# Optimization experiments

Hardware: AMD Instinct MI355X
Metric: run time of the kernel (lower is better)

The kernel has to match this reference:

```python
import jax, jax.numpy as jnp
import numpy as np

TOP_K = 2


def setup_inputs() -> dict:
    key = jax.random.key(0)
    k0, k1, k2, k3 = jax.random.split(key, 4)
    B, T, C, E, D = 4, 2048, 1024, 8, 1024  # D = 4*C*top_k//E
    x = jax.random.normal(k0, (B, T, C), dtype=jnp.float32)
    s = 1.0 / np.sqrt(C)
    w_router = jax.random.normal(k1, (C, E), dtype=jnp.float32) * s
    w1 = jax.random.normal(k2, (E, C, D), dtype=jnp.float32) * s  # c_fc.weight.T per expert
    w2 = jax.random.normal(k3, (E, D, C), dtype=jnp.float32) * (1.0 / np.sqrt(D))  # c_proj.weight.T
    return {"x": x, "w_router": w_router, "w1": w1, "w2": w2}


def reference(x, w_router, w1, w2):
    B, T, C = x.shape
    xf = x.reshape(-1, C)  # [N, C]
    logits = xf @ w_router  # [N, E]
    top_vals, top_idx = jax.lax.top_k(logits, TOP_K)  # [N, k]
    probs = jax.nn.softmax(top_vals, axis=-1)  # softmax over selected experts only
    # Dense per-expert MLP (relu^2), identical math to per-token weight gather:
    h = jnp.square(jax.nn.relu(jnp.einsum('nc,ecd->ned', xf, w1)))  # [N, E, D]
    y_all = jnp.einsum('ned,edc->nec', h, w2)  # [N, E, C]
    y_sel = jnp.take_along_axis(y_all, top_idx[:, :, None], axis=1)  # [N, k, C]
    out = jnp.sum(y_sel * probs[:, :, None], axis=1)  # [N, C]
    return out.reshape(B, T, C)
```

## Files before the change

kernel.cpp:

```cpp
#include <hip/hip_runtime.h>
#include <stdint.h>

typedef unsigned short u16;
typedef unsigned int u32;

constexpr int C = 1024;
constexpr int E = 8;
constexpr int D = 1024;
constexpr int BM = 128, BN = 128, BK = 32;

typedef short s16x8 __attribute__((ext_vector_type(8)));
typedef float f32x4 __attribute__((ext_vector_type(4)));

__device__ __forceinline__ u16 f2bf(float f) {
  union { float f; u32 u; } v; v.f = f;
  return (u16)((v.u + 0x7FFFu + ((v.u >> 16) & 1u)) >> 16);
}
__device__ __forceinline__ float bf2f(u32 u) {
  union { u32 u; float f; } v; v.u = u << 16; return v.f;
}

typedef __attribute__((address_space(1))) const u32 gu32;
typedef __attribute__((address_space(3))) u32 lu32;
__device__ __forceinline__ void gl_lds16(const void* g, void* l) {
  __builtin_amdgcn_global_load_lds((gu32*)g, (lu32*)l, 16, 0, 0);
}
template <int N>
__device__ __forceinline__ void waitvm() {
  asm volatile("s_waitcnt vmcnt(%0)" :: "i"(N) : "memory");
  __builtin_amdgcn_sched_barrier(0);
}
__device__ __forceinline__ void bar() {
  __builtin_amdgcn_s_barrier();
  __builtin_amdgcn_sched_barrier(0);
}

__global__ void __launch_bounds__(256) k_wt(const float* __restrict__ w1,
                                            const float* __restrict__ w2,
                                            u16* __restrict__ w1t, u16* __restrict__ w2t,
                                            const float* __restrict__ wr,
                                            float* __restrict__ wrT,
                                            int* __restrict__ ints) {
  int b = blockIdx.x;
  int t = threadIdx.x;
  if (b >= 4096) {
    if (t < 64) ints[t] = 0;
    for (int g = t; g < C * E; g += 256) wrT[(g & 7) * C + (g >> 3)] = wr[g];
    return;
  }
  __shared__ float tile[64][65];
  int which = b >> 11;
  int rem = b & 2047;
  int e = rem >> 8, kt = (rem >> 4) & 15, nt = rem & 15;
  const float* src = (which ? w2 : w1) + (size_t)e * C * D;
  u16* dst = (which ? w2t : w1t) + (size_t)e * C * D;
#pragma unroll
  for (int i = 0; i < 4; ++i) {
    int lin = i * 256 + t;
    int r = lin >> 4, c4 = lin & 15;
    f32x4 v = *(const f32x4*)(src + (size_t)(kt * 64 + r) * 1024 + nt * 64 + c4 * 4);
    tile[r][c4 * 4 + 0] = v[0]; tile[r][c4 * 4 + 1] = v[1];
    tile[r][c4 * 4 + 2] = v[2]; tile[r][c4 * 4 + 3] = v[3];
  }
  __syncthreads();
#pragma unroll
  for (int i = 0; i < 2; ++i) {
    int lin = i * 256 + t;
    int nr = lin >> 3, k8 = lin & 7;
    u32 o[4];
#pragma unroll
    for (int j = 0; j < 4; ++j)
      o[j] = (u32)f2bf(tile[k8 * 8 + 2 * j][nr]) |
             ((u32)f2bf(tile[k8 * 8 + 2 * j + 1][nr]) << 16);
    *(uint4*)(dst + (size_t)(nt * 64 + nr) * 1024 + kt * 64 + k8 * 8) = *(const uint4*)o;
  }
}

__global__ void __launch_bounds__(256) k_router(const float* __restrict__ x,
                                                const float* __restrict__ wrT,
                                                u16* __restrict__ xb,
                                                int* __restrict__ tok_e,
                                                float* __restrict__ tok_p,
                                                int* __restrict__ counts) {
  __shared__ float lg[32][9];
  __shared__ int cl[8];
  int t = threadIdx.x;
  int tok0 = blockIdx.x * 32;
  int tl = t >> 3, e = t & 7;
  if (t < 8) cl[t] = 0;
  size_t tok = (size_t)tok0 + tl;
  const f32x4* xr = (const f32x4*)(x + tok * C);
  const f32x4* wv4 = (const f32x4*)(wrT + e * C);
  float a0 = 0.f, a1 = 0.f, a2 = 0.f, a3 = 0.f;
#pragma unroll 4
  for (int i = 0; i < C / 4; ++i) {
    f32x4 xv = xr[i], wv = wv4[i];
    a0 += xv[0] * wv[0]; a1 += xv[1] * wv[1];
    a2 += xv[2] * wv[2]; a3 += xv[3] * wv[3];
  }
  lg[tl][e] = (a0 + a1) + (a2 + a3);
  __syncthreads();
  if (t < 32) {
    int myTok = tok0 + t;
    float v0 = -1e30f; int i0 = 0;
#pragma unroll
    for (int q = 0; q < 8; ++q) { float v = lg[t][q]; if (v > v0) { v0 = v; i0 = q; } }
    float v1 = -1e30f; int i1 = 0;
#pragma unroll
    for (int q = 0; q < 8; ++q) {
      if (q == i0) continue;
      float v = lg[t][q]; if (v > v1) { v1 = v; i1 = q; }
    }
    float dd = expf(v1 - v0);
    float s = 1.f / (1.f + dd);
    tok_e[myTok * 2 + 0] = i0; tok_e[myTok * 2 + 1] = i1;
    tok_p[myTok * 2 + 0] = s;  tok_p[myTok * 2 + 1] = dd * s;
    atomicAdd(&cl[i0], 1); atomicAdd(&cl[i1], 1);
  }
  __syncthreads();
  if (t < 8 && cl[t] > 0) atomicAdd(&counts[t], cl[t]);
  const f32x4* xall = (const f32x4*)(x + (size_t)tok0 * C);
  uint2* xb2 = (uint2*)(xb + (size_t)tok0 * C);
  for (int i = t; i < 32 * C / 4; i += 256) {
    f32x4 v = xall[i];
    uint2 o;
    o.x = (u32)f2bf(v[0]) | ((u32)f2bf(v[1]) << 16);
    o.y = (u32)f2bf(v[2]) | ((u32)f2bf(v[3]) << 16);
    xb2[i] = o;
  }
}

__global__ void __launch_bounds__(256) k_build(const int* __restrict__ tok_e,
                                               const int* __restrict__ counts,
                                               int* __restrict__ cnt2,
                                               int* __restrict__ offs,
                                               int* __restrict__ list_tok,
                                               int* __restrict__ inv) {
  int gid = blockIdx.x * 256 + threadIdx.x;
  int offv[9]; int off = 0;
#pragma unroll
  for (int q = 0; q < 8; ++q) { offv[q] = off; off += (counts[q] + (BM - 1)) & ~(BM - 1); }
  offv[8] = off;
  if (blockIdx.x == 0 && threadIdx.x < 9) offs[threadIdx.x] = offv[threadIdx.x];
  int lane = threadIdx.x & 63;
#pragma unroll
  for (int s = 0; s < 2; ++s) {
    int e = tok_e[gid * 2 + s];
    for (int q = 0; q < 8; ++q) {
      unsigned long long mask = __ballot(e == q);
      if (mask == 0ull) continue;
      int leader = __ffsll(mask) - 1;
      int cnt = __popcll(mask);
      int base = 0;
      if (lane == leader) base = atomicAdd(&cnt2[q], cnt);
      base = __shfl(base, leader, 64);
      if (e == q) {
        int pos = offv[q] + base + __popcll(mask & ((1ull << lane) - 1ull));
        list_tok[pos] = gid;
        inv[gid * 2 + s] = pos;
      }
    }
  }
}

template <int MODE>
__global__ void __launch_bounds__(256, 4) k_gemm(const u16* __restrict__ A,
                                                 const u16* __restrict__ Bt,
                                                 u16* __restrict__ Hout,
                                                 const int* __restrict__ list_tok,
                                                 const int* __restrict__ offs,
                                                 int Ntok) {
  __shared__ u16 A0[BM * BK], B0[BN * BK], A1[BM * BK], B1[BN * BK];
  int b = blockIdx.x;
  int nper = gridDim.x >> 3;
  int logical = (b & 7) * nper + (b >> 3);
  int m0 = (logical >> 3) * BM;
  int n0 = (logical & 7) * BN;
  if (m0 >= offs[8]) return;
  int e = 0;
#pragma unroll
  for (int q = 1; q < 8; ++q) e += (m0 >= offs[q]);

  int t = threadIdx.x;
  int l = t & 63, w = t >> 6;
  int wm = w >> 1, wn = w & 1;

  const u16* ag[2]; const u16* bg[2];
#pragma unroll
  for (int j = 0; j < 2; ++j) {
    int row = w * 32 + j * 16 + (l >> 2);
    int coff = (((l & 3) ^ ((row >> 1) & 3)) << 3);
    if (MODE == 0) {
      int tk = list_tok[m0 + row];
      tk = (tk < 0 || tk >= Ntok) ? 0 : tk;
      ag[j] = A + (size_t)tk * C + coff;
    } else {
      ag[j] = A + (size_t)(m0 + row) * C + coff;
    }
    bg[j] = Bt + (size_t)e * C * D + (size_t)(n0 + row) * 1024 + coff;
  }
  u16* a0 = &A0[w * 1024]; u16* b0 = &B0[w * 1024];
  u16* a1 = &A1[w * 1024]; u16* b1 = &B1[w * 1024];

  f32x4 acc[4][4];
#pragma unroll
  for (int m = 0; m < 4; ++m)
#pragma unroll
    for (int n = 0; n < 4; ++n) acc[m][n] = (f32x4){0.f, 0.f, 0.f, 0.f};

  auto STAGE = [&](int k0, u16* al, u16* bl) {
#pragma unroll
    for (int j = 0; j < 2; ++j) {
      gl_lds16(ag[j] + k0, al + j * 512);
      gl_lds16(bg[j] + k0, bl + j * 512);
    }
  };
  auto COMPUTE = [&](const u16* Al, const u16* Bl) {
    s16x8 af[4], bf[4];
    int cr = l >> 4;
#pragma unroll
    for (int m = 0; m < 4; ++m) {
      int row = wm * 64 + m * 16 + (l & 15);
      af[m] = *(const s16x8*)&Al[row * BK + ((cr ^ ((row >> 1) & 3)) << 3)];
    }
#pragma unroll
    for (int n = 0; n < 4; ++n) {
      int row = wn * 64 + n * 16 + (l & 15);
      bf[n] = *(const s16x8*)&Bl[row * BK + ((cr ^ ((row >> 1) & 3)) << 3)];
    }
#pragma unroll
    for (int m = 0; m < 4; ++m)
#pragma unroll
      for (int n = 0; n < 4; ++n)
        acc[m][n] = __builtin_amdgcn_mfma_f32_16x16x32_bf16(af[m], bf[n], acc[m][n], 0, 0, 0);
  };

  STAGE(0, a0, b0);
  STAGE(BK, a1, b1);
#pragma unroll 1
  for (int tt = 0; tt < 32; tt += 2) {
    waitvm<4>();
    bar();
    COMPUTE(A0, B0);
    bar();
    if (tt + 2 < 32) STAGE((tt + 2) * BK, a0, b0);
    if (tt + 2 < 32) waitvm<4>(); else waitvm<0>();
    bar();
    COMPUTE(A1, B1);
    bar();
    if (tt + 3 < 32) STAGE((tt + 3) * BK, a1, b1);
  }

#pragma unroll
  for (int m = 0; m < 4; ++m) {
#pragma unroll
    for (int r = 0; r < 4; ++r) {
      int grow = m0 + wm * 64 + m * 16 + ((l >> 4) << 2) + r;
      u16* hp = Hout + (size_t)grow * 1024 + n0 + wn * 64 + (l & 15);
#pragma unroll
      for (int n = 0; n < 4; ++n) {
        float v = acc[m][n][r];
        if (MODE == 0) { v = fmaxf(v, 0.f); v = v * v; }
        hp[n * 16] = f2bf(v);
      }
    }
  }
}

__global__ void __launch_bounds__(256) k_combine(const u16* __restrict__ Y,
                                                 const int* __restrict__ inv,
                                                 const float* __restrict__ tok_p,
                                                 float* __restrict__ out) {
  int gid = blockIdx.x * 4 + (threadIdx.x >> 6);
  int l = threadIdx.x & 63;
  int s0 = inv[gid * 2 + 0], s1 = inv[gid * 2 + 1];
  float p0 = tok_p[gid * 2 + 0], p1 = tok_p[gid * 2 + 1];
  const uint4* y0 = (const uint4*)(Y + (size_t)s0 * 1024);
  const uint4* y1 = (const uint4*)(Y + (size_t)s1 * 1024);
  f32x4* o = (f32x4*)(out + (size_t)gid * 1024);
#pragma unroll
  for (int i = 0; i < 2; ++i) {
    int c = i * 64 + l;
    uint4 a = y0[c], bb = y1[c];
    f32x4 r0, r1;
    r0[0] = p0 * bf2f(a.x & 0xffffu) + p1 * bf2f(bb.x & 0xffffu);
    r0[1] = p0 * bf2f(a.x >> 16)     + p1 * bf2f(bb.x >> 16);
    r0[2] = p0 * bf2f(a.y & 0xffffu) + p1 * bf2f(bb.y & 0xffffu);
    r0[3] = p0 * bf2f(a.y >> 16)     + p1 * bf2f(bb.y >> 16);
    r1[0] = p0 * bf2f(a.z & 0xffffu) + p1 * bf2f(bb.z & 0xffffu);
    r1[1] = p0 * bf2f(a.z >> 16)     + p1 * bf2f(bb.z >> 16);
    r1[2] = p0 * bf2f(a.w & 0xffffu) + p1 * bf2f(bb.w & 0xffffu);
    r1[3] = p0 * bf2f(a.w >> 16)     + p1 * bf2f(bb.w >> 16);
    o[c * 2 + 0] = r0;
    o[c * 2 + 1] = r1;
  }
}

extern "C" void kernel_launch(void* const* d_in, const int* in_sizes, int n_in,
                              void* d_out, int out_size, void* d_ws, size_t ws_size,
                              hipStream_t stream) {
  const float* x  = (const float*)d_in[0];
  const float* wr = (const float*)d_in[1];
  const float* w1 = (const float*)d_in[2];
  const float* w2 = (const float*)d_in[3];
  float* out = (float*)d_out;
  const int Ntok = in_sizes[0] / C;
  const int ROWS = 2 * Ntok + E * BM;

  char* p = (char*)d_ws;
  u16* xb  = (u16*)p; p += (size_t)Ntok * C * 2;
  u16* w1t = (u16*)p; p += (size_t)E * C * D * 2;
  u16* w2t = (u16*)p; p += (size_t)E * C * D * 2;
  u16* h   = (u16*)p; p += (size_t)ROWS * D * 2;
  u16* y   = (u16*)p; p += (size_t)ROWS * C * 2;
  float* wrT = (float*)p; p += (size_t)C * E * 4;
  int* list_tok = (int*)p; p += (size_t)ROWS * 4;
  int* inv = (int*)p; p += (size_t)Ntok * 2 * 4;
  int* tok_e = (int*)p; p += (size_t)Ntok * 2 * 4;
  float* tok_p = (float*)p; p += (size_t)Ntok * 2 * 4;
  int* ints = (int*)p; p += 256;
  int* counts = ints;
  int* offs = ints + 16;
  int* cnt2 = ints + 32;
  (void)ws_size; (void)n_in; (void)out_size;

  k_wt<<<4097, 256, 0, stream>>>(w1, w2, w1t, w2t, wr, wrT, ints);
  k_router<<<Ntok / 32, 256, 0, stream>>>(x, wrT, xb, tok_e, tok_p, counts);
  k_build<<<Ntok / 256, 256, 0, stream>>>(tok_e, counts, cnt2, offs, list_tok, inv);
  k_gemm<0><<<(ROWS / BM) * 8, 256, 0, stream>>>(xb, w1t, h, list_tok, offs, Ntok);
  k_gemm<1><<<(ROWS / BM) * 8, 256, 0, stream>>>(h, w2t, y, list_tok, offs, Ntok);
  k_combine<<<Ntok / 4, 256, 0, stream>>>(y, inv, tok_p, out);
}
```

Before: 208.2 us.

## Triple-buffer GEMM LDS pipeline and move x bf16 conversion into weight-transpose kernel

```diff
diff --git a/kernel.cpp b/kernel.cpp
--- a/kernel.cpp
+++ b/kernel.cpp
@@ -40,10 +40,26 @@
                                             u16* __restrict__ w1t, u16* __restrict__ w2t,
                                             const float* __restrict__ wr,
                                             float* __restrict__ wrT,
-                                            int* __restrict__ ints) {
+                                            int* __restrict__ ints,
+                                            const float* __restrict__ x,
+                                            u16* __restrict__ xb, int Ntok) {
   int b = blockIdx.x;
   int t = threadIdx.x;
-  if (b >= 4096) {
+  if (b > 4096) {
+    int xbid = b - 4097;
+    const f32x4* src = (const f32x4*)x;
+    uint2* dst = (uint2*)xb;
+    int total = Ntok * (C / 4);
+    for (int i = xbid * 256 + t; i < total; i += 1024 * 256) {
+      f32x4 v = src[i];
+      uint2 o;
+      o.x = (u32)f2bf(v[0]) | ((u32)f2bf(v[1]) << 16);
+      o.y = (u32)f2bf(v[2]) | ((u32)f2bf(v[3]) << 16);
+      dst[i] = o;
+    }
+    return;
+  }
+  if (b == 4096) {
     if (t < 64) ints[t] = 0;
     for (int g = t; g < C * E; g += 256) wrT[(g & 7) * C + (g >> 3)] = wr[g];
     return;
@@ -78,7 +94,6 @@
 
 __global__ void __launch_bounds__(256) k_router(const float* __restrict__ x,
                                                 const float* __restrict__ wrT,
-                                                u16* __restrict__ xb,
                                                 int* __restrict__ tok_e,
                                                 float* __restrict__ tok_p,
                                                 int* __restrict__ counts) {
@@ -119,15 +134,6 @@
   }
   __syncthreads();
   if (t < 8 && cl[t] > 0) atomicAdd(&counts[t], cl[t]);
-  const f32x4* xall = (const f32x4*)(x + (size_t)tok0 * C);
-  uint2* xb2 = (uint2*)(xb + (size_t)tok0 * C);
-  for (int i = t; i < 32 * C / 4; i += 256) {
-    f32x4 v = xall[i];
-    uint2 o;
-    o.x = (u32)f2bf(v[0]) | ((u32)f2bf(v[1]) << 16);
-    o.y = (u32)f2bf(v[2]) | ((u32)f2bf(v[3]) << 16);
-    xb2[i] = o;
-  }
 }
 
 __global__ void __launch_bounds__(256) k_build(const int* __restrict__ tok_e,
@@ -164,13 +170,13 @@
 }
 
 template <int MODE>
-__global__ void __launch_bounds__(256, 4) k_gemm(const u16* __restrict__ A,
+__global__ void __launch_bounds__(256, 3) k_gemm(const u16* __restrict__ A,
                                                  const u16* __restrict__ Bt,
                                                  u16* __restrict__ Hout,
                                                  const int* __restrict__ list_tok,
                                                  const int* __restrict__ offs,
                                                  int Ntok) {
-  __shared__ u16 A0[BM * BK], B0[BN * BK], A1[BM * BK], B1[BN * BK];
+  __shared__ u16 A0[BM * BK], B0[BN * BK], A1[BM * BK], B1[BN * BK], A2[BM * BK], B2[BN * BK];
   int b = blockIdx.x;
   int nper = gridDim.x >> 3;
   int logical = (b & 7) * nper + (b >> 3);
@@ -201,6 +207,7 @@
   }
   u16* a0 = &A0[w * 1024]; u16* b0 = &B0[w * 1024];
   u16* a1 = &A1[w * 1024]; u16* b1 = &B1[w * 1024];
+  u16* a2 = &A2[w * 1024]; u16* b2 = &B2[w * 1024];
 
   f32x4 acc[4][4];
 #pragma unroll
@@ -228,28 +235,25 @@
       int row = wn * 64 + n * 16 + (l & 15);
       bf[n] = *(const s16x8*)&Bl[row * BK + ((cr ^ ((row >> 1) & 3)) << 3)];
     }
+    __builtin_amdgcn_s_setprio(1);
 #pragma unroll
     for (int m = 0; m < 4; ++m)
 #pragma unroll
       for (int n = 0; n < 4; ++n)
         acc[m][n] = __builtin_amdgcn_mfma_f32_16x16x32_bf16(af[m], bf[n], acc[m][n], 0, 0, 0);
+    __builtin_amdgcn_s_setprio(0);
   };
 
   STAGE(0, a0, b0);
   STAGE(BK, a1, b1);
 #pragma unroll 1
-  for (int tt = 0; tt < 32; tt += 2) {
-    waitvm<4>();
-    bar();
-    COMPUTE(A0, B0);
-    bar();
-    if (tt + 2 < 32) STAGE((tt + 2) * BK, a0, b0);
-    if (tt + 2 < 32) waitvm<4>(); else waitvm<0>();
-    bar();
-    COMPUTE(A1, B1);
-    bar();
-    if (tt + 3 < 32) STAGE((tt + 3) * BK, a1, b1);
-  }
+  for (int tt = 0; tt < 30; tt += 3) {
+    STAGE((tt + 2) * BK, a2, b2); waitvm<8>(); bar(); COMPUTE(A0, B0); bar();
+    STAGE((tt + 3) * BK, a0, b0); waitvm<8>(); bar(); COMPUTE(A1, B1); bar();
+    STAGE((tt + 4) * BK, a1, b1); waitvm<8>(); bar(); COMPUTE(A2, B2); bar();
+  }
+  waitvm<4>(); bar(); COMPUTE(A0, B0);
+  waitvm<0>(); bar(); COMPUTE(A1, B1);
 
 #pragma unroll
   for (int m = 0; m < 4; ++m) {
@@ -324,8 +328,8 @@
   int* cnt2 = ints + 32;
   (void)ws_size; (void)n_in; (void)out_size;
 
-  k_wt<<<4097, 256, 0, stream>>>(w1, w2, w1t, w2t, wr, wrT, ints);
-  k_router<<<Ntok / 32, 256, 0, stream>>>(x, wrT, xb, tok_e, tok_p, counts);
+  k_wt<<<4097 + 1024, 256, 0, stream>>>(w1, w2, w1t, w2t, wr, wrT, ints, x, xb, Ntok);
+  k_router<<<Ntok / 32, 256, 0, stream>>>(x, wrT, tok_e, tok_p, counts);
   k_build<<<Ntok / 256, 256, 0, stream>>>(tok_e, counts, cnt2, offs, list_tok, inv);
   k_gemm<0><<<(ROWS / BM) * 8, 256, 0, stream>>>(xb, w1t, h, list_tok, offs, Ntok);
   k_gemm<1><<<(ROWS / BM) * 8, 256, 0, stream>>>(h, w2t, y, list_tok, offs, Ntok);
```

Measured after the change: 202.1 us. 1.03x faster.

## Overlap w2 conversion with first GEMM and triple-buffer GEMM LDS pipeline

Applied to the files above, without the earlier changes.

```diff
diff --git a/kernel.cpp b/kernel.cpp
--- a/kernel.cpp
+++ b/kernel.cpp
@@ -36,24 +36,21 @@
 }
 
 __global__ void __launch_bounds__(256) k_wt(const float* __restrict__ w1,
-                                            const float* __restrict__ w2,
-                                            u16* __restrict__ w1t, u16* __restrict__ w2t,
+                                            u16* __restrict__ w1t,
                                             const float* __restrict__ wr,
                                             float* __restrict__ wrT,
                                             int* __restrict__ ints) {
   int b = blockIdx.x;
   int t = threadIdx.x;
-  if (b >= 4096) {
+  if (b >= 2048) {
     if (t < 64) ints[t] = 0;
     for (int g = t; g < C * E; g += 256) wrT[(g & 7) * C + (g >> 3)] = wr[g];
     return;
   }
   __shared__ float tile[64][65];
-  int which = b >> 11;
-  int rem = b & 2047;
-  int e = rem >> 8, kt = (rem >> 4) & 15, nt = rem & 15;
-  const float* src = (which ? w2 : w1) + (size_t)e * C * D;
-  u16* dst = (which ? w2t : w1t) + (size_t)e * C * D;
+  int e = b >> 8, kt = (b >> 4) & 15, nt = b & 15;
+  const float* src = w1 + (size_t)e * C * D;
+  u16* dst = w1t + (size_t)e * C * D;
 #pragma unroll
   for (int i = 0; i < 4; ++i) {
     int lin = i * 256 + t;
@@ -164,15 +161,49 @@
 }
 
 template <int MODE>
-__global__ void __launch_bounds__(256, 4) k_gemm(const u16* __restrict__ A,
+__global__ void __launch_bounds__(256, 3) k_gemm(const u16* __restrict__ A,
                                                  const u16* __restrict__ Bt,
                                                  u16* __restrict__ Hout,
                                                  const int* __restrict__ list_tok,
                                                  const int* __restrict__ offs,
-                                                 int Ntok) {
-  __shared__ u16 A0[BM * BK], B0[BN * BK], A1[BM * BK], B1[BN * BK];
+                                                 int Ntok,
+                                                 const float* __restrict__ Wf,
+                                                 u16* __restrict__ Wt) {
+  __shared__ u16 S[6][4096];
   int b = blockIdx.x;
-  int nper = gridDim.x >> 3;
+  int Ggemm = (MODE == 0) ? ((int)gridDim.x - 2048) : (int)gridDim.x;
+
+  if (MODE == 0 && b >= Ggemm) {
+    int b2 = b - Ggemm;
+    int t = threadIdx.x;
+    float (*tile)[65] = (float (*)[65])&S[0][0];
+    int e2 = b2 >> 8, kt = (b2 >> 4) & 15, nt = b2 & 15;
+    const float* src = Wf + (size_t)e2 * C * D;
+    u16* dst = Wt + (size_t)e2 * C * D;
+#pragma unroll
+    for (int i = 0; i < 4; ++i) {
+      int lin = i * 256 + t;
+      int r = lin >> 4, c4 = lin & 15;
+      f32x4 v = *(const f32x4*)(src + (size_t)(kt * 64 + r) * 1024 + nt * 64 + c4 * 4);
+      tile[r][c4 * 4 + 0] = v[0]; tile[r][c4 * 4 + 1] = v[1];
+      tile[r][c4 * 4 + 2] = v[2]; tile[r][c4 * 4 + 3] = v[3];
+    }
+    __syncthreads();
+#pragma unroll
+    for (int i = 0; i < 2; ++i) {
+      int lin = i * 256 + t;
+      int nr = lin >> 3, k8 = lin & 7;
+      u32 o[4];
+#pragma unroll
+      for (int j = 0; j < 4; ++j)
+        o[j] = (u32)f2bf(tile[k8 * 8 + 2 * j][nr]) |
+               ((u32)f2bf(tile[k8 * 8 + 2 * j + 1][nr]) << 16);
+      *(uint4*)(dst + (size_t)(nt * 64 + nr) * 1024 + kt * 64 + k8 * 8) = *(const uint4*)o;
+    }
+    return;
+  }
+
+  int nper = Ggemm >> 3;
   int logical = (b & 7) * nper + (b >> 3);
   int m0 = (logical >> 3) * BM;
   int n0 = (logical & 7) * BN;
@@ -199,8 +230,9 @@
     }
     bg[j] = Bt + (size_t)e * C * D + (size_t)(n0 + row) * 1024 + coff;
   }
-  u16* a0 = &A0[w * 1024]; u16* b0 = &B0[w * 1024];
-  u16* a1 = &A1[w * 1024]; u16* b1 = &B1[w * 1024];
+  u16* a0 = &S[0][w * 1024]; u16* b0 = &S[1][w * 1024];
+  u16* a1 = &S[2][w * 1024]; u16* b1 = &S[3][w * 1024];
+  u16* a2 = &S[4][w * 1024]; u16* b2 = &S[5][w * 1024];
 
   f32x4 acc[4][4];
 #pragma unroll
@@ -228,28 +260,25 @@
       int row = wn * 64 + n * 16 + (l & 15);
       bf[n] = *(const s16x8*)&Bl[row * BK + ((cr ^ ((row >> 1) & 3)) << 3)];
     }
+    __builtin_amdgcn_s_setprio(1);
 #pragma unroll
     for (int m = 0; m < 4; ++m)
 #pragma unroll
       for (int n = 0; n < 4; ++n)
         acc[m][n] = __builtin_amdgcn_mfma_f32_16x16x32_bf16(af[m], bf[n], acc[m][n], 0, 0, 0);
+    __builtin_amdgcn_s_setprio(0);
   };
 
   STAGE(0, a0, b0);
   STAGE(BK, a1, b1);
 #pragma unroll 1
-  for (int tt = 0; tt < 32; tt += 2) {
-    waitvm<4>();
-    bar();
-    COMPUTE(A0, B0);
-    bar();
-    if (tt + 2 < 32) STAGE((tt + 2) * BK, a0, b0);
-    if (tt + 2 < 32) waitvm<4>(); else waitvm<0>();
-    bar();
-    COMPUTE(A1, B1);
-    bar();
-    if (tt + 3 < 32) STAGE((tt + 3) * BK, a1, b1);
-  }
+  for (int tt = 0; tt < 30; tt += 3) {
+    STAGE((tt + 2) * BK, a2, b2); waitvm<8>(); bar(); COMPUTE(S[0], S[1]); bar();
+    STAGE((tt + 3) * BK, a0, b0); waitvm<8>(); bar(); COMPUTE(S[2], S[3]); bar();
+    STAGE((tt + 4) * BK, a1, b1); waitvm<8>(); bar(); COMPUTE(S[4], S[5]); bar();
+  }
+  waitvm<4>(); bar(); COMPUTE(S[0], S[1]);
+  waitvm<0>(); bar(); COMPUTE(S[2], S[3]);
 
 #pragma unroll
   for (int m = 0; m < 4; ++m) {
@@ -306,6 +335,7 @@
   float* out = (float*)d_out;
   const int Ntok = in_sizes[0] / C;
   const int ROWS = 2 * Ntok + E * BM;
+  const int G = (ROWS / BM) * 8;
 
   char* p = (char*)d_ws;
   u16* xb  = (u16*)p; p += (size_t)Ntok * C * 2;
@@ -324,10 +354,10 @@
   int* cnt2 = ints + 32;
   (void)ws_size; (void)n_in; (void)out_size;
 
-  k_wt<<<4097, 256, 0, stream>>>(w1, w2, w1t, w2t, wr, wrT, ints);
+  k_wt<<<2049, 256, 0, stream>>>(w1, w1t, wr, wrT, ints);
   k_router<<<Ntok / 32, 256, 0, stream>>>(x, wrT, xb, tok_e, tok_p, counts);
   k_build<<<Ntok / 256, 256, 0, stream>>>(tok_e, counts, cnt2, offs, list_tok, inv);
-  k_gemm<0><<<(ROWS / BM) * 8, 256, 0, stream>>>(xb, w1t, h, list_tok, offs, Ntok);
-  k_gemm<1><<<(ROWS / BM) * 8, 256, 0, stream>>>(h, w2t, y, list_tok, offs, Ntok);
+  k_gemm<0><<<G + 2048, 256, 0, stream>>>(xb, w1t, h, list_tok, offs, Ntok, w2, w2t);
+  k_gemm<1><<<G, 256, 0, stream>>>(h, w2t, y, list_tok, offs, Ntok, nullptr, nullptr);
   k_combine<<<Ntok / 4, 256, 0, stream>>>(y, inv, tok_p, out);
 }
```

Measured after the change: 201.7 us. 1.03x faster.
